# Kernel tuning notes

Measured on AMD Instinct MI355X. Metric: run time of the kernel, lower is better.

Reference implementation:

```python
import jax, jax.numpy as jnp
import numpy as np

B, N, D = 4, 2048, 256
H = 8
HD = D // H
FF = 1024
EPS = 1e-5


def layer_norm(x, g, b):
    mu = jnp.mean(x, axis=-1, keepdims=True)
    var = jnp.mean((x - mu) ** 2, axis=-1, keepdims=True)
    return (x - mu) * jax.lax.rsqrt(var + EPS) * g + b


def setup_inputs() -> dict:
    key = jax.random.key(0)
    ks = jax.random.split(key, 12)
    s = 0.02
    return {
        "tokens": jax.random.normal(ks[0], (B, N, D), dtype=jnp.float32),
        "key_padding_mask": jnp.zeros((B, N), dtype=bool),
        "ln1_g": jnp.ones((D,), jnp.float32),
        "ln1_b": jnp.zeros((D,), jnp.float32),
        "wq": jax.random.normal(ks[1], (D, D), jnp.float32) * s,
        "bq": jnp.zeros((D,), jnp.float32),
        "wk": jax.random.normal(ks[2], (D, D), jnp.float32) * s,
        "bk": jnp.zeros((D,), jnp.float32),
        "wv": jax.random.normal(ks[3], (D, D), jnp.float32) * s,
        "bv": jnp.zeros((D,), jnp.float32),
        "wo": jax.random.normal(ks[4], (D, D), jnp.float32) * s,
        "bo": jnp.zeros((D,), jnp.float32),
        "ln2_g": jnp.ones((D,), jnp.float32),
        "ln2_b": jnp.zeros((D,), jnp.float32),
        "w1": jax.random.normal(ks[5], (D, FF), jnp.float32) * s,
        "b1": jnp.zeros((FF,), jnp.float32),
        "w2": jax.random.normal(ks[6], (FF, D), jnp.float32) * s,
        "b2": jnp.zeros((D,), jnp.float32),
    }


def reference(tokens, key_padding_mask, ln1_g, ln1_b, wq, bq, wk, bk, wv, bv,
              wo, bo, ln2_g, ln2_b, w1, b1, w2, b2):
    x = tokens
    # --- self-attention sublayer (pre-LN) ---
    xn = layer_norm(x, ln1_g, ln1_b)
    q = (xn @ wq + bq).reshape(B, N, H, HD).transpose(0, 2, 1, 3)  # [B,H,N,HD]
    k = (xn @ wk + bk).reshape(B, N, H, HD).transpose(0, 2, 1, 3)
    v = (xn @ wv + bv).reshape(B, N, H, HD).transpose(0, 2, 1, 3)
    scores = jnp.einsum('bhqd,bhkd->bhqk', q, k) / np.sqrt(HD).astype(np.float32)
    scores = jnp.where(key_padding_mask[:, None, None, :], -jnp.inf, scores)
    probs = jax.nn.softmax(scores, axis=-1)
    attn = jnp.einsum('bhqk,bhkd->bhqd', probs, v)
    attn = attn.transpose(0, 2, 1, 3).reshape(B, N, D)
    x = x + (attn @ wo + bo)
    # --- feed-forward sublayer (pre-LN) ---
    xn2 = layer_norm(x, ln2_g, ln2_b)
    h = jax.nn.gelu(xn2 @ w1 + b1, approximate=False)  # torch GELU is exact erf
    x = x + (h @ w2 + b2)
    return x
```

## Files before the change

kernel.cpp:

```cpp
#include <hip/hip_runtime.h>
#include <cmath>

typedef __attribute__((ext_vector_type(8))) __bf16 bf16x8;
typedef __attribute__((ext_vector_type(4))) __bf16 bf16x4;
typedef __attribute__((ext_vector_type(4))) float  f32x4;

constexpr int NB   = 4;
constexpr int SEQ  = 2048;
constexpr int DM   = 256;
constexpr int NH   = 8;
constexpr int DH   = 32;
constexpr int DFF  = 1024;
constexpr int MTOK = NB * SEQ;

__global__ __launch_bounds__(256) void ln_kernel(const float* __restrict__ x,
                                                 const float* __restrict__ g,
                                                 const float* __restrict__ b,
                                                 __bf16* __restrict__ out) {
  int wave = threadIdx.x >> 6, lane = threadIdx.x & 63;
  int row = blockIdx.x * 4 + wave;
  const float* xr = x + (size_t)row * DM;
  f32x4 v = *(const f32x4*)(xr + lane * 4);
  float s  = v[0] + v[1] + v[2] + v[3];
  float sq = v[0]*v[0] + v[1]*v[1] + v[2]*v[2] + v[3]*v[3];
  #pragma unroll
  for (int off = 1; off < 64; off <<= 1) {
    s  += __shfl_xor(s, off);
    sq += __shfl_xor(sq, off);
  }
  float mu  = s * (1.0f / DM);
  float var = sq * (1.0f / DM) - mu * mu;
  float rs  = rsqrtf(var + 1e-5f);
  f32x4 gv = *(const f32x4*)(g + lane * 4);
  f32x4 bv = *(const f32x4*)(b + lane * 4);
  bf16x4 o;
  #pragma unroll
  for (int i = 0; i < 4; ++i) o[i] = (__bf16)((v[i] - mu) * rs * gv[i] + bv[i]);
  *(bf16x4*)(out + (size_t)row * DM + lane * 4) = o;
}

__global__ __launch_bounds__(256) void prep_kernel(
    const float* __restrict__ wq, const float* __restrict__ wk, const float* __restrict__ wv,
    const float* __restrict__ wo, const float* __restrict__ w1, const float* __restrict__ w2,
    const unsigned char* __restrict__ mask, const float* __restrict__ tokens,
    const float* __restrict__ ln1g, const float* __restrict__ ln1b,
    __bf16* __restrict__ wqkvT, __bf16* __restrict__ woT,
    __bf16* __restrict__ w1T, __bf16* __restrict__ w2T,
    float* __restrict__ madd_g, __bf16* __restrict__ xn1) {
  __shared__ float tile[32][33];
  int bid = blockIdx.x;
  int tid = threadIdx.x;
  if (bid >= 800) {
    int row = (bid - 800) * 4 + (tid >> 6);
    int lane = tid & 63;
    const float* xr = tokens + (size_t)row * DM;
    f32x4 v = *(const f32x4*)(xr + lane * 4);
    float s  = v[0] + v[1] + v[2] + v[3];
    float sq = v[0]*v[0] + v[1]*v[1] + v[2]*v[2] + v[3]*v[3];
    #pragma unroll
    for (int off = 1; off < 64; off <<= 1) {
      s  += __shfl_xor(s, off);
      sq += __shfl_xor(sq, off);
    }
    float mu  = s * (1.0f / DM);
    float var = sq * (1.0f / DM) - mu * mu;
    float rs  = rsqrtf(var + 1e-5f);
    f32x4 gv = *(const f32x4*)(ln1g + lane * 4);
    f32x4 bv = *(const f32x4*)(ln1b + lane * 4);
    bf16x4 o;
    #pragma unroll
    for (int i = 0; i < 4; ++i) o[i] = (__bf16)((v[i] - mu) * rs * gv[i] + bv[i]);
    *(bf16x4*)(xn1 + (size_t)row * DM + lane * 4) = o;
    return;
  }
  if (bid >= 768) {
    int idx = (bid - 768) * 256 + tid;
    madd_g[idx] = mask[idx] ? -__builtin_inff() : 0.0f;
    return;
  }
  const float* W; __bf16* Wt; int K, N, n0, k0;
  if (bid < 256) {
    int z = bid >> 6, local = bid & 63;
    K = 256; N = 256;
    n0 = (local & 7) * 32; k0 = (local >> 3) * 32;
    if      (z == 0) { W = wq; Wt = wqkvT;          }
    else if (z == 1) { W = wk; Wt = wqkvT + 65536;  }
    else if (z == 2) { W = wv; Wt = wqkvT + 131072; }
    else             { W = wo; Wt = woT;            }
  } else if (bid < 512) {
    int local = bid - 256;
    W = w1; Wt = w1T; K = 256; N = 1024;
    n0 = (local & 31) * 32; k0 = (local >> 5) * 32;
  } else {
    int local = bid - 512;
    W = w2; Wt = w2T; K = 1024; N = 256;
    n0 = (local & 7) * 32; k0 = (local >> 3) * 32;
  }
  {
    int kl = tid >> 3, n4 = (tid & 7) * 4;
    f32x4 v = *(const f32x4*)(W + (size_t)(k0 + kl) * N + n0 + n4);
    tile[kl][n4 + 0] = v[0]; tile[kl][n4 + 1] = v[1];
    tile[kl][n4 + 2] = v[2]; tile[kl][n4 + 3] = v[3];
  }
  __syncthreads();
  {
    int nl = tid >> 3, k4 = (tid & 7) * 4;
    bf16x4 o;
    #pragma unroll
    for (int i = 0; i < 4; ++i) o[i] = (__bf16)tile[k4 + i][nl];
    *(bf16x4*)(Wt + (size_t)(n0 + nl) * K + k0 + k4) = o;
  }
}

template<int BM, int BN, int EP, int AF = 0>
__global__ __launch_bounds__(256) void gemm_bt(
    const __bf16* __restrict__ A, const __bf16* __restrict__ Bt,
    int M, int N, int K,
    const float* __restrict__ bias,
    const float* __restrict__ bq, const float* __restrict__ bk, const float* __restrict__ bv,
    const float* __restrict__ resid, float* __restrict__ outf,
    __bf16* __restrict__ outb,
    __bf16* __restrict__ outq, __bf16* __restrict__ outk, __bf16* __restrict__ outv,
    const float* __restrict__ Af = nullptr, const float* __restrict__ lpart = nullptr) {
  constexpr int MT = BM / 32, NT = BN / 32;
  constexpr int AP = BM / 32, BP = BN / 32;
  __shared__ __bf16 As[BM * 64];
  __shared__ __bf16 Bs[BN * 64];
  int tid = threadIdx.x;
  int wave = tid >> 6, lane = tid & 63;
  int wm = wave >> 1, wn = wave & 1;
  int quad = lane >> 4, l16 = lane & 15;
  int m0 = blockIdx.x * BM, n0 = blockIdx.y * BN;
  int lrow = lane >> 3;
  int lcg  = ((lane & 7) ^ lrow) * 8;

  auto loadA = [&](int rbase, int kcol) -> bf16x8 {
    int gr = m0 + rbase + lrow;
    if constexpr (AF == 0) {
      return *(const bf16x8*)(A + (size_t)gr * K + kcol);
    } else {
      const float* p0 = Af + (size_t)gr * K + kcol;
      const float* p1 = p0 + (size_t)MTOK * DM;
      f32x4 a0 = *(const f32x4*)p0, a0b = *(const f32x4*)(p0 + 4);
      f32x4 a1 = *(const f32x4*)p1, a1b = *(const f32x4*)(p1 + 4);
      int bb = gr >> 11, tok = gr & 2047, hh = kcol >> 5;
      float l = lpart[((size_t)bb * NH + hh) * SEQ + tok] +
                lpart[(((size_t)NB + bb) * NH + hh) * SEQ + tok];
      float inv = 1.0f / l;
      bf16x8 o;
      #pragma unroll
      for (int i = 0; i < 4; ++i) {
        o[i]     = (__bf16)((a0[i]  + a1[i])  * inv);
        o[i + 4] = (__bf16)((a0b[i] + a1b[i]) * inv);
      }
      return o;
    }
  };

  f32x4 acc[MT][NT];
  #pragma unroll
  for (int mt = 0; mt < MT; ++mt)
    #pragma unroll
    for (int nt = 0; nt < NT; ++nt)
      #pragma unroll
      for (int r = 0; r < 4; ++r) acc[mt][nt][r] = 0.0f;

  bf16x8 ap[AP], bp[BP];
  #pragma unroll
  for (int i = 0; i < AP; ++i) ap[i] = loadA(wave * (BM / 4) + i * 8, lcg);
  #pragma unroll
  for (int i = 0; i < BP; ++i) {
    int rbase = wave * (BN / 4) + i * 8;
    bp[i] = *(const bf16x8*)(Bt + (size_t)(n0 + rbase + lrow) * K + lcg);
  }
  #pragma unroll
  for (int i = 0; i < AP; ++i) {
    int rbase = wave * (BM / 4) + i * 8;
    *(bf16x8*)&As[rbase * 64 + lane * 8] = ap[i];
  }
  #pragma unroll
  for (int i = 0; i < BP; ++i) {
    int rbase = wave * (BN / 4) + i * 8;
    *(bf16x8*)&Bs[rbase * 64 + lane * 8] = bp[i];
  }
  __syncthreads();

  for (int kt = 0; kt < K; kt += 64) {
    bool more = (kt + 64) < K;
    if (more) {
      #pragma unroll
      for (int i = 0; i < AP; ++i) ap[i] = loadA(wave * (BM / 4) + i * 8, kt + 64 + lcg);
      #pragma unroll
      for (int i = 0; i < BP; ++i) {
        int rbase = wave * (BN / 4) + i * 8;
        bp[i] = *(const bf16x8*)(Bt + (size_t)(n0 + rbase + lrow) * K + kt + 64 + lcg);
      }
    }
    #pragma unroll
    for (int ks = 0; ks < 2; ++ks) {
      bf16x8 af[MT], bfr[NT];
      #pragma unroll
      for (int mt = 0; mt < MT; ++mt) {
        int row = wm * (BM / 2) + mt * 16 + l16;
        af[mt] = *(const bf16x8*)&As[row * 64 + (((ks * 4 + quad) ^ (l16 & 7)) * 8)];
      }
      #pragma unroll
      for (int nt = 0; nt < NT; ++nt) {
        int row = wn * (BN / 2) + nt * 16 + l16;
        bfr[nt] = *(const bf16x8*)&Bs[row * 64 + (((ks * 4 + quad) ^ (l16 & 7)) * 8)];
      }
      #pragma unroll
      for (int mt = 0; mt < MT; ++mt)
        #pragma unroll
        for (int nt = 0; nt < NT; ++nt)
          acc[mt][nt] = __builtin_amdgcn_mfma_f32_16x16x32_bf16(af[mt], bfr[nt], acc[mt][nt], 0, 0, 0);
    }
    if (more) {
      __syncthreads();
      #pragma unroll
      for (int i = 0; i < AP; ++i) {
        int rbase = wave * (BM / 4) + i * 8;
        *(bf16x8*)&As[rbase * 64 + lane * 8] = ap[i];
      }
      #pragma unroll
      for (int i = 0; i < BP; ++i) {
        int rbase = wave * (BN / 4) + i * 8;
        *(bf16x8*)&Bs[rbase * 64 + lane * 8] = bp[i];
      }
      __syncthreads();
    }
  }

  #pragma unroll
  for (int mt = 0; mt < MT; ++mt)
  #pragma unroll
  for (int nt = 0; nt < NT; ++nt)
  #pragma unroll
  for (int r = 0; r < 4; ++r) {
    int gm = m0 + wm * (BM / 2) + mt * 16 + quad * 4 + r;
    int gn = n0 + wn * (BN / 2) + nt * 16 + l16;
    float v = acc[mt][nt][r];
    if constexpr (EP == 0) {
      int which = gn >> 8, nn = gn & 255;
      const float* bp2 = which == 0 ? bq : (which == 1 ? bk : bv);
      v += bp2[nn];
      int h = nn >> 5, hd = nn & 31;
      int bb = gm >> 11, tok = gm & 2047;
      if (which == 2) {
        outv[(((size_t)(bb * NH + h)) * DH + hd) * SEQ + tok] = (__bf16)v;
      } else {
        __bf16* dst = which == 0 ? outq : outk;
        dst[(((size_t)(bb * NH + h)) * SEQ + tok) * DH + hd] = (__bf16)v;
      }
    } else if constexpr (EP == 1) {
      v += bias[gn] + resid[(size_t)gm * N + gn];
      outf[(size_t)gm * N + gn] = v;
    } else {
      v += bias[gn];
      float v2 = v * v;
      float t = __builtin_amdgcn_exp2f(v * (2.3022082f + 0.10294324f * v2));
      outb[(size_t)gm * N + gn] = (__bf16)(v * t * __builtin_amdgcn_rcpf(t + 1.0f));
    }
  }
}

__global__ __launch_bounds__(256) void attn_kernel(
    const __bf16* __restrict__ Q, const __bf16* __restrict__ K,
    const __bf16* __restrict__ Vt, const float* __restrict__ madd_g,
    float* __restrict__ Opart, float* __restrict__ lpart) {
  constexpr float C2 = 0.2550350030061664f;
  __shared__ __bf16 Ks[128][36];
  __shared__ __bf16 Vs[32][132];
  __shared__ __bf16 Ps[4][2][16][68];
  int bh = blockIdx.x;
  int q0 = blockIdx.y * 128;
  int half = blockIdx.z;
  int b  = bh >> 3, h = bh & 7;
  int tid = threadIdx.x;
  int wave = tid >> 6, lane = tid & 63;
  int quad = lane >> 4, l16 = lane & 15;
  const __bf16* Qb = Q  + (size_t)bh * SEQ * DH;
  const __bf16* Kb = K  + (size_t)bh * SEQ * DH;
  const __bf16* Vb = Vt + (size_t)bh * DH * SEQ;
  const float* maddb = madd_g + b * SEQ;
  int qw = q0 + wave * 32;
  int kbase = half * (SEQ / 2);

  bf16x8 qf[2];
  #pragma unroll
  for (int qg = 0; qg < 2; ++qg)
    qf[qg] = *(const bf16x8*)(Qb + (size_t)(qw + qg * 16 + l16) * DH + quad * 8);

  bf16x8 ones;
  #pragma unroll
  for (int i = 0; i < 8; ++i) ones[i] = (__bf16)1.0f;

  f32x4 o[2][2], ol[2];
  #pragma unroll
  for (int qg = 0; qg < 2; ++qg) {
    #pragma unroll
    for (int nt = 0; nt < 2; ++nt)
      #pragma unroll
      for (int r = 0; r < 4; ++r) o[qg][nt][r] = 0.0f;
    #pragma unroll
    for (int r = 0; r < 4; ++r) ol[qg][r] = 0.0f;
  }

  f32x4 zf; zf[0] = zf[1] = zf[2] = zf[3] = 0.0f;

  for (int st = 0; st < 8; ++st) {
    int kb0 = kbase + st * 128;
    __syncthreads();
    #pragma unroll
    for (int p = 0; p < 2; ++p) {
      int c = p * 256 + tid, row = c >> 2, cg = (c & 3) * 8;
      *(bf16x8*)&Ks[row][cg] = *(const bf16x8*)(Kb + (size_t)(kb0 + row) * DH + cg);
    }
    #pragma unroll
    for (int p = 0; p < 2; ++p) {
      int c = p * 256 + tid, row = c >> 4, cg = (c & 15) * 8;
      *(bf16x8*)&Vs[row][cg] = *(const bf16x8*)(Vb + (size_t)row * SEQ + kb0 + cg);
    }
    __syncthreads();

    #pragma unroll
    for (int sub = 0; sub < 2; ++sub) {
      int kl = sub * 64;
      f32x4 s[2][4];
      #pragma unroll
      for (int mt = 0; mt < 4; ++mt) {
        bf16x8 kf = *(const bf16x8*)&Ks[kl + mt * 16 + l16][quad * 8];
        s[0][mt] = __builtin_amdgcn_mfma_f32_16x16x32_bf16(kf, qf[0], zf, 0, 0, 0);
        s[1][mt] = __builtin_amdgcn_mfma_f32_16x16x32_bf16(kf, qf[1], zf, 0, 0, 0);
      }
      #pragma unroll
      for (int mt = 0; mt < 4; ++mt) {
        f32x4 md = *(const f32x4*)(maddb + kb0 + kl + mt * 16 + quad * 4);
        #pragma unroll
        for (int qg = 0; qg < 2; ++qg) {
          bf16x4 pv;
          #pragma unroll
          for (int r = 0; r < 4; ++r)
            pv[r] = (__bf16)__builtin_amdgcn_exp2f(fmaf(s[qg][mt][r], C2, md[r]));
          *(bf16x4*)&Ps[wave][qg][l16][mt * 16 + quad * 4] = pv;
        }
      }
      #pragma unroll
      for (int ks = 0; ks < 2; ++ks) {
        bf16x8 vf[2];
        #pragma unroll
        for (int nt = 0; nt < 2; ++nt)
          vf[nt] = *(const bf16x8*)&Vs[nt * 16 + l16][kl + ks * 32 + quad * 8];
        #pragma unroll
        for (int qg = 0; qg < 2; ++qg) {
          bf16x8 pf = *(const bf16x8*)&Ps[wave][qg][l16][ks * 32 + quad * 8];
          #pragma unroll
          for (int nt = 0; nt < 2; ++nt)
            o[qg][nt] = __builtin_amdgcn_mfma_f32_16x16x32_bf16(pf, vf[nt], o[qg][nt], 0, 0, 0);
          ol[qg] = __builtin_amdgcn_mfma_f32_16x16x32_bf16(pf, ones, ol[qg], 0, 0, 0);
        }
      }
    }
  }

  float* Op = Opart + (size_t)half * MTOK * DM;
  #pragma unroll
  for (int qg = 0; qg < 2; ++qg) {
    #pragma unroll
    for (int nt = 0; nt < 2; ++nt)
      #pragma unroll
      for (int r = 0; r < 4; ++r) {
        int q   = qw + qg * 16 + quad * 4 + r;
        int col = h * DH + nt * 16 + l16;
        Op[((size_t)(b * SEQ + q)) * DM + col] = o[qg][nt][r];
      }
    if (l16 == 0) {
      #pragma unroll
      for (int r = 0; r < 4; ++r)
        lpart[((((size_t)half * NB + b) * NH) + h) * SEQ + qw + qg * 16 + quad * 4 + r] = ol[qg][r];
    }
  }
}

extern "C" void kernel_launch(void* const* d_in, const int* in_sizes, int n_in,
                              void* d_out, int out_size, void* d_ws, size_t ws_size,
                              hipStream_t stream) {
  const float* tokens = (const float*)d_in[0];
  const unsigned char* mask = (const unsigned char*)d_in[1];
  const float* ln1g = (const float*)d_in[2];
  const float* ln1b = (const float*)d_in[3];
  const float* wq = (const float*)d_in[4];
  const float* bq = (const float*)d_in[5];
  const float* wk = (const float*)d_in[6];
  const float* bk = (const float*)d_in[7];
  const float* wv = (const float*)d_in[8];
  const float* bv = (const float*)d_in[9];
  const float* wo = (const float*)d_in[10];
  const float* bo = (const float*)d_in[11];
  const float* ln2g = (const float*)d_in[12];
  const float* ln2b = (const float*)d_in[13];
  const float* w1 = (const float*)d_in[14];
  const float* b1 = (const float*)d_in[15];
  const float* w2 = (const float*)d_in[16];
  const float* b2 = (const float*)d_in[17];
  float* out = (float*)d_out;
  char* ws = (char*)d_ws;

  __bf16* wqkvT = (__bf16*)(ws + 0);
  __bf16* woT   = (__bf16*)(ws + 393216);
  __bf16* w1T   = (__bf16*)(ws + 524288);
  __bf16* w2T   = (__bf16*)(ws + 1048576);
  __bf16* xn1   = (__bf16*)(ws + 1572864);
  float*  lpart = (float*)(ws + 1572864);
  __bf16* qb    = (__bf16*)(ws + 5767168);
  __bf16* kb    = (__bf16*)(ws + 9961472);
  __bf16* vt    = (__bf16*)(ws + 18350080);
  float*  x1    = (float*)(ws + 26738688);
  __bf16* xn2   = (__bf16*)(ws + 35127296);
  __bf16* hbuf  = (__bf16*)(ws + 39321600);
  float*  Opart = (float*)(ws + 39321600);
  float*  madd  = (float*)(ws + 56098816);

  prep_kernel<<<2848, 256, 0, stream>>>(
      wq, wk, wv, wo, w1, w2, mask, tokens, ln1g, ln1b,
      wqkvT, woT, w1T, w2T, madd, xn1);

  gemm_bt<128, 64, 0><<<dim3(64, 12), 256, 0, stream>>>(
      xn1, wqkvT, MTOK, 768, 256, nullptr, bq, bk, bv,
      nullptr, nullptr, nullptr, qb, kb, vt);

  attn_kernel<<<dim3(32, SEQ / 128, 2), 256, 0, stream>>>(qb, kb, vt, madd, Opart, lpart);

  gemm_bt<64, 64, 1, 1><<<dim3(128, 4), 256, 0, stream>>>(
      nullptr, woT, MTOK, 256, 256, bo, nullptr, nullptr, nullptr,
      tokens, x1, nullptr, nullptr, nullptr, nullptr, Opart, lpart);

  ln_kernel<<<MTOK / 4, 256, 0, stream>>>(x1, ln2g, ln2b, xn2);

  gemm_bt<128, 128, 2><<<dim3(64, 8), 256, 0, stream>>>(
      xn2, w1T, MTOK, DFF, 256, b1, nullptr, nullptr, nullptr,
      nullptr, nullptr, hbuf, nullptr, nullptr, nullptr);

  gemm_bt<64, 64, 1><<<dim3(128, 4), 256, 0, stream>>>(
      hbuf, w2T, MTOK, 256, DFF, b2, nullptr, nullptr, nullptr,
      x1, out, nullptr, nullptr, nullptr, nullptr);
}
```

Measured before the change: 188.8 us.

## Add register-resident B-fragment GEMM without LDS for K=256 projections

Introduces gemm_regb, where each wave keeps a 32-column slice of the transposed weight (full K=256) in registers and streams 32-row A tiles straight from global memory into MFMA, with no shared memory or barriers. The QKV, output-projection and FFN1 GEMMs switch to this kernel, while FFN2 (K=1024) keeps the LDS-tiled gemm_bt, which is reduced to the residual epilogue. The goal is to remove LDS staging and sync overhead for these short-K GEMMs. In exchange, A rows are reloaded by every N-slice wave instead of shared through LDS, and reads of 16 rows per fragment are less coalesced, so global and L2 traffic goes up.

```diff
diff --git a/kernel.cpp b/kernel.cpp
--- a/kernel.cpp
+++ b/kernel.cpp
@@ -112,16 +112,122 @@
   }
 }
 
-template<int BM, int BN, int EP, int AF = 0>
+template<int EP, int MITERS>
+__global__ __launch_bounds__(256) void gemm_regb(
+    const __bf16* __restrict__ A, const __bf16* __restrict__ Bt, int N,
+    const float* __restrict__ bias,
+    const float* __restrict__ bq, const float* __restrict__ bk, const float* __restrict__ bv,
+    const float* __restrict__ resid, float* __restrict__ outf, __bf16* __restrict__ outb,
+    __bf16* __restrict__ outq, __bf16* __restrict__ outk, __bf16* __restrict__ outv,
+    const float* __restrict__ Af, const float* __restrict__ lpart) {
+  constexpr int KD = 256, KS = 8;
+  int wglob = blockIdx.x * 4 + (threadIdx.x >> 6);
+  int lane = threadIdx.x & 63;
+  int quad = lane >> 4, l16 = lane & 15;
+  int nslices = N >> 5;
+  int nsl = wglob % nslices;
+  int mch = wglob / nslices;
+  int n0 = nsl * 32;
+
+  bf16x8 bfrag[2][KS];
+  #pragma unroll
+  for (int nt = 0; nt < 2; ++nt)
+    #pragma unroll
+    for (int ks = 0; ks < KS; ++ks)
+      bfrag[nt][ks] = *(const bf16x8*)(Bt + (size_t)(n0 + nt * 16 + l16) * KD + ks * 32 + quad * 8);
+
+  #pragma unroll
+  for (int it = 0; it < MITERS; ++it) {
+    int m0 = (mch * MITERS + it) * 32;
+
+    bf16x8 af[2][KS];
+    if constexpr (EP == 1) {
+      #pragma unroll
+      for (int am = 0; am < 2; ++am) {
+        int gr = m0 + am * 16 + l16;
+        int bb = gr >> 11, tok = gr & 2047;
+        #pragma unroll
+        for (int ks = 0; ks < KS; ++ks) {
+          const float* p0 = Af + (size_t)gr * KD + ks * 32 + quad * 8;
+          const float* p1 = p0 + (size_t)MTOK * DM;
+          f32x4 a0 = *(const f32x4*)p0, a0b = *(const f32x4*)(p0 + 4);
+          f32x4 a1 = *(const f32x4*)p1, a1b = *(const f32x4*)(p1 + 4);
+          float l = lpart[((size_t)bb * NH + ks) * SEQ + tok] +
+                    lpart[(((size_t)NB + bb) * NH + ks) * SEQ + tok];
+          float inv = 1.0f / l;
+          bf16x8 o;
+          #pragma unroll
+          for (int i = 0; i < 4; ++i) {
+            o[i]     = (__bf16)((a0[i]  + a1[i])  * inv);
+            o[i + 4] = (__bf16)((a0b[i] + a1b[i]) * inv);
+          }
+          af[am][ks] = o;
+        }
+      }
+    } else {
+      #pragma unroll
+      for (int am = 0; am < 2; ++am)
+        #pragma unroll
+        for (int ks = 0; ks < KS; ++ks)
+          af[am][ks] = *(const bf16x8*)(A + (size_t)(m0 + am * 16 + l16) * KD + ks * 32 + quad * 8);
+    }
+
+    f32x4 acc[2][2];
+    #pragma unroll
+    for (int am = 0; am < 2; ++am)
+      #pragma unroll
+      for (int nt = 0; nt < 2; ++nt)
+        #pragma unroll
+        for (int r = 0; r < 4; ++r) acc[am][nt][r] = 0.0f;
+
+    #pragma unroll
+    for (int ks = 0; ks < KS; ++ks)
+      #pragma unroll
+      for (int am = 0; am < 2; ++am)
+        #pragma unroll
+        for (int nt = 0; nt < 2; ++nt)
+          acc[am][nt] = __builtin_amdgcn_mfma_f32_16x16x32_bf16(af[am][ks], bfrag[nt][ks], acc[am][nt], 0, 0, 0);
+
+    #pragma unroll
+    for (int am = 0; am < 2; ++am)
+    #pragma unroll
+    for (int nt = 0; nt < 2; ++nt)
+    #pragma unroll
+    for (int r = 0; r < 4; ++r) {
+      int gm = m0 + am * 16 + quad * 4 + r;
+      int gn = n0 + nt * 16 + l16;
+      float v = acc[am][nt][r];
+      if constexpr (EP == 0) {
+        int which = gn >> 8, nn = gn & 255;
+        const float* bp2 = which == 0 ? bq : (which == 1 ? bk : bv);
+        v += bp2[nn];
+        int h = nn >> 5, hd = nn & 31;
+        int bb = gm >> 11, tok = gm & 2047;
+        if (which == 2) {
+          outv[(((size_t)(bb * NH + h)) * DH + hd) * SEQ + tok] = (__bf16)v;
+        } else {
+          __bf16* dst = which == 0 ? outq : outk;
+          dst[(((size_t)(bb * NH + h)) * SEQ + tok) * DH + hd] = (__bf16)v;
+        }
+      } else if constexpr (EP == 1) {
+        v += bias[gn] + resid[(size_t)gm * DM + gn];
+        outf[(size_t)gm * DM + gn] = v;
+      } else {
+        v += bias[gn];
+        float v2 = v * v;
+        float t = __builtin_amdgcn_exp2f(v * (2.3022082f + 0.10294324f * v2));
+        outb[(size_t)gm * N + gn] = (__bf16)(v * t * __builtin_amdgcn_rcpf(t + 1.0f));
+      }
+    }
+  }
+}
+
+template<int BM, int BN, int EP>
 __global__ __launch_bounds__(256) void gemm_bt(
     const __bf16* __restrict__ A, const __bf16* __restrict__ Bt,
     int M, int N, int K,
     const float* __restrict__ bias,
-    const float* __restrict__ bq, const float* __restrict__ bk, const float* __restrict__ bv,
-    const float* __restrict__ resid, float* __restrict__ outf,
-    __bf16* __restrict__ outb,
-    __bf16* __restrict__ outq, __bf16* __restrict__ outk, __bf16* __restrict__ outv,
-    const float* __restrict__ Af = nullptr, const float* __restrict__ lpart = nullptr) {
+    const float* __restrict__ resid, float* __restrict__ outf) {
   constexpr int MT = BM / 32, NT = BN / 32;
   constexpr int AP = BM / 32, BP = BN / 32;
   __shared__ __bf16 As[BM * 64];
@@ -134,29 +240,6 @@
   int lrow = lane >> 3;
   int lcg  = ((lane & 7) ^ lrow) * 8;
 
-  auto loadA = [&](int rbase, int kcol) -> bf16x8 {
-    int gr = m0 + rbase + lrow;
-    if constexpr (AF == 0) {
-      return *(const bf16x8*)(A + (size_t)gr * K + kcol);
-    } else {
-      const float* p0 = Af + (size_t)gr * K + kcol;
-      const float* p1 = p0 + (size_t)MTOK * DM;
-      f32x4 a0 = *(const f32x4*)p0, a0b = *(const f32x4*)(p0 + 4);
-      f32x4 a1 = *(const f32x4*)p1, a1b = *(const f32x4*)(p1 + 4);
-      int bb = gr >> 11, tok = gr & 2047, hh = kcol >> 5;
-      float l = lpart[((size_t)bb * NH + hh) * SEQ + tok] +
-                lpart[(((size_t)NB + bb) * NH + hh) * SEQ + tok];
-      float inv = 1.0f / l;
-      bf16x8 o;
-      #pragma unroll
-      for (int i = 0; i < 4; ++i) {
-        o[i]     = (__bf16)((a0[i]  + a1[i])  * inv);
-        o[i + 4] = (__bf16)((a0b[i] + a1b[i]) * inv);
-      }
-      return o;
-    }
-  };
-
   f32x4 acc[MT][NT];
   #pragma unroll
   for (int mt = 0; mt < MT; ++mt)
@@ -167,7 +250,10 @@
 
   bf16x8 ap[AP], bp[BP];
   #pragma unroll
-  for (int i = 0; i < AP; ++i) ap[i] = loadA(wave * (BM / 4) + i * 8, lcg);
+  for (int i = 0; i < AP; ++i) {
+    int rbase = wave * (BM / 4) + i * 8;
+    ap[i] = *(const bf16x8*)(A + (size_t)(m0 + rbase + lrow) * K + lcg);
+  }
   #pragma unroll
   for (int i = 0; i < BP; ++i) {
     int rbase = wave * (BN / 4) + i * 8;
@@ -189,7 +275,10 @@
     bool more = (kt + 64) < K;
     if (more) {
       #pragma unroll
-      for (int i = 0; i < AP; ++i) ap[i] = loadA(wave * (BM / 4) + i * 8, kt + 64 + lcg);
+      for (int i = 0; i < AP; ++i) {
+        int rbase = wave * (BM / 4) + i * 8;
+        ap[i] = *(const bf16x8*)(A + (size_t)(m0 + rbase + lrow) * K + kt + 64 + lcg);
+      }
       #pragma unroll
       for (int i = 0; i < BP; ++i) {
         int rbase = wave * (BN / 4) + i * 8;
@@ -239,28 +328,8 @@
   for (int r = 0; r < 4; ++r) {
     int gm = m0 + wm * (BM / 2) + mt * 16 + quad * 4 + r;
     int gn = n0 + wn * (BN / 2) + nt * 16 + l16;
-    float v = acc[mt][nt][r];
-    if constexpr (EP == 0) {
-      int which = gn >> 8, nn = gn & 255;
-      const float* bp2 = which == 0 ? bq : (which == 1 ? bk : bv);
-      v += bp2[nn];
-      int h = nn >> 5, hd = nn & 31;
-      int bb = gm >> 11, tok = gm & 2047;
-      if (which == 2) {
-        outv[(((size_t)(bb * NH + h)) * DH + hd) * SEQ + tok] = (__bf16)v;
-      } else {
-        __bf16* dst = which == 0 ? outq : outk;
-        dst[(((size_t)(bb * NH + h)) * SEQ + tok) * DH + hd] = (__bf16)v;
-      }
-    } else if constexpr (EP == 1) {
-      v += bias[gn] + resid[(size_t)gm * N + gn];
-      outf[(size_t)gm * N + gn] = v;
-    } else {
-      v += bias[gn];
-      float v2 = v * v;
-      float t = __builtin_amdgcn_exp2f(v * (2.3022082f + 0.10294324f * v2));
-      outb[(size_t)gm * N + gn] = (__bf16)(v * t * __builtin_amdgcn_rcpf(t + 1.0f));
-    }
+    float v = acc[mt][nt][r] + bias[gn] + resid[(size_t)gm * N + gn];
+    outf[(size_t)gm * N + gn] = v;
   }
 }
 
@@ -425,23 +494,22 @@
       wq, wk, wv, wo, w1, w2, mask, tokens, ln1g, ln1b,
       wqkvT, woT, w1T, w2T, madd, xn1);
 
-  gemm_bt<128, 64, 0><<<dim3(64, 12), 256, 0, stream>>>(
-      xn1, wqkvT, MTOK, 768, 256, nullptr, bq, bk, bv,
-      nullptr, nullptr, nullptr, qb, kb, vt);
+  gemm_regb<0, 2><<<768, 256, 0, stream>>>(
+      xn1, wqkvT, 768, nullptr, bq, bk, bv,
+      nullptr, nullptr, nullptr, qb, kb, vt, nullptr, nullptr);
 
   attn_kernel<<<dim3(32, SEQ / 128, 2), 256, 0, stream>>>(qb, kb, vt, madd, Opart, lpart);
 
-  gemm_bt<64, 64, 1, 1><<<dim3(128, 4), 256, 0, stream>>>(
-      nullptr, woT, MTOK, 256, 256, bo, nullptr, nullptr, nullptr,
+  gemm_regb<1, 1><<<512, 256, 0, stream>>>(
+      nullptr, woT, 256, bo, nullptr, nullptr, nullptr,
       tokens, x1, nullptr, nullptr, nullptr, nullptr, Opart, lpart);
 
   ln_kernel<<<MTOK / 4, 256, 0, stream>>>(x1, ln2g, ln2b, xn2);
 
-  gemm_bt<128, 128, 2><<<dim3(64, 8), 256, 0, stream>>>(
-      xn2, w1T, MTOK, DFF, 256, b1, nullptr, nullptr, nullptr,
-      nullptr, nullptr, hbuf, nullptr, nullptr, nullptr);
+  gemm_regb<2, 2><<<1024, 256, 0, stream>>>(
+      xn2, w1T, 1024, b1, nullptr, nullptr, nullptr,
+      nullptr, nullptr, hbuf, nullptr, nullptr, nullptr, nullptr, nullptr);
 
   gemm_bt<64, 64, 1><<<dim3(128, 4), 256, 0, stream>>>(
-      hbuf, w2T, MTOK, 256, DFF, b2, nullptr, nullptr, nullptr,
-      x1, out, nullptr, nullptr, nullptr, nullptr);
+      hbuf, w2T, MTOK, 256, DFF, b2, x1, out);
 }
```

Result: slower. 228.1 us (+20.8%).
